# Performance work log

Hardware: AMD Instinct MI355X
Metric: run time of the kernel (lower is better)

Reference implementation:

```python
import jax, jax.numpy as jnp
import numpy as np

IN_FEATURES = 4096
OUT_FEATURES = 4096
N_OUTLIERS = 40
NBITS = 8


def setup_inputs() -> dict:
    key = jax.random.key(0)
    k1, k2, k3, k4 = jax.random.split(key, 4)
    x = jax.random.normal(k1, (4, 2048, IN_FEATURES), dtype=jnp.float32)
    weight = jax.random.normal(k2, (OUT_FEATURES, IN_FEATURES), dtype=jnp.float32)
    B = jax.random.normal(k3, (OUT_FEATURES, N_OUTLIERS), dtype=jnp.float32)
    bias = jax.random.normal(k4, (1, OUT_FEATURES), dtype=jnp.float32)
    # evenly spread outlier channel indices (as from_float would pick hot channels)
    outlier_idx = (jnp.arange(N_OUTLIERS, dtype=jnp.int32) * 102).astype(jnp.int32)
    return {"x": x, "weight": weight, "B": B, "bias": bias, "outlier_idx": outlier_idx}


def _uniform_quant(t, n_bits=NBITS):
    q_max = 2 ** (n_bits - 1) - 1  # 127 for 8 bits
    scale = jnp.maximum(jnp.max(jnp.abs(t)), 1e-5) / q_max
    return jnp.round(t / scale) * scale


def reference(x, weight, B, bias, outlier_idx):
    # abs-max over non-outlier channels only (mask out outlier columns)
    mask = jnp.ones((IN_FEATURES,), dtype=x.dtype).at[outlier_idx].set(0.0)
    upper = jnp.max(jnp.abs(x) * mask)
    x_clip = jnp.clip(x, -upper, upper)
    # outlier residual: part of x clipped away on the outlier channels
    x_outlier = jnp.take(x, outlier_idx, axis=-1) - jnp.take(x_clip, outlier_idx, axis=-1)
    res_y = jnp.einsum('bsk,ok->bso', x_outlier, B)  # skinny GEMM [*,40] x [40,out]
    # fake-quantize clipped activations, then main GEMM
    q_x = _uniform_quant(x_clip)
    y = jnp.einsum('bsi,oi->bso', q_x, weight) + bias
    # quantize_output=False -> no_quant on y
    return y + res_y
```

## Files before the change

kernel.cpp:

```cpp
#include <hip/hip_runtime.h>
#include <hip/hip_bf16.h>
#include <stdint.h>

#define IN_F 4096
#define OUT_F 4096
#define NOUT 40
#define KPAD 4160
#define M_TOT 8192

#define BM 256
#define BN 256
#define BK 64
#define KTILES 65

typedef float f32x4 __attribute__((ext_vector_type(4)));
typedef __bf16 bf16x8 __attribute__((ext_vector_type(8)));

typedef __attribute__((address_space(1))) void GV;
typedef __attribute__((address_space(3))) void LV;
#define GLDS16(gp, lp) \
  __builtin_amdgcn_global_load_lds((GV*)(gp), (LV*)(lp), 16, 0, 0)

__device__ __forceinline__ unsigned short f2bf(float f) {
  unsigned u = __float_as_uint(f);
  u += 0x7FFFu + ((u >> 16) & 1u);
  return (unsigned short)(u >> 16);
}

__global__ void k_absmax(const float4* __restrict__ x4, const int* __restrict__ oidx,
                         unsigned* __restrict__ out) {
  __shared__ unsigned bits[128];
  const int t = threadIdx.x;
  if (t < 128) bits[t] = 0;
  __syncthreads();
  if (t < NOUT) {
    int c = oidx[t];
    atomicOr(&bits[c >> 5], 1u << (c & 31));
  }
  __syncthreads();
  const int n4 = M_TOT * IN_F / 4;
  float m = 0.f;
  const int stride = gridDim.x * blockDim.x;
  for (int i = blockIdx.x * blockDim.x + t; i < n4; i += stride) {
    float4 u = x4[i];
    unsigned wb = bits[(i & 1023) >> 3];
    int sh = (i & 7) * 4;
    m = fmaxf(m, ((wb >> (sh + 0)) & 1) ? 0.f : fabsf(u.x));
    m = fmaxf(m, ((wb >> (sh + 1)) & 1) ? 0.f : fabsf(u.y));
    m = fmaxf(m, ((wb >> (sh + 2)) & 1) ? 0.f : fabsf(u.z));
    m = fmaxf(m, ((wb >> (sh + 3)) & 1) ? 0.f : fabsf(u.w));
  }
#pragma unroll
  for (int off = 32; off; off >>= 1) m = fmaxf(m, __shfl_down(m, off, 64));
  if ((t & 63) == 0) atomicMax(out, __float_as_uint(m));
}

__global__ void k_prep_a(const float* __restrict__ x,
                         const int* __restrict__ oidx,
                         const unsigned* __restrict__ upper_bits,
                         unsigned short* __restrict__ A) {
  const int m = blockIdx.x;
  const int t = threadIdx.x;
  const float upper = __uint_as_float(*upper_bits);
  const float inv = 127.0f / fmaxf(upper, 1e-5f);
  const float4* xr = (const float4*)(x + (size_t)m * IN_F);
  uint4* Ar = (uint4*)(A + (size_t)m * KPAD);
#pragma unroll
  for (int rep = 0; rep < 2; ++rep) {
    const int c = t + rep * 256;
    float4 u0 = xr[2 * c];
    float4 u1 = xr[2 * c + 1];
    float f[8] = {u0.x, u0.y, u0.z, u0.w, u1.x, u1.y, u1.z, u1.w};
    unsigned o[4];
#pragma unroll
    for (int w = 0; w < 4; ++w) {
      float a = fminf(fmaxf(f[2 * w], -upper), upper);
      float b = fminf(fmaxf(f[2 * w + 1], -upper), upper);
      unsigned short b0 = f2bf(rintf(a * inv));
      unsigned short b1 = f2bf(rintf(b * inv));
      o[w] = (unsigned)b0 | ((unsigned)b1 << 16);
    }
    uint4 ov; ov.x = o[0]; ov.y = o[1]; ov.z = o[2]; ov.w = o[3];
    Ar[c] = ov;
  }
  if (t < 64) {
    unsigned short v = 0;
    if (t < NOUT) {
      float xf = x[(size_t)m * IN_F + oidx[t]];
      float xc = fminf(fmaxf(xf, -upper), upper);
      v = f2bf((xf - xc) * inv);
    }
    A[(size_t)m * KPAD + IN_F + t] = v;
  }
}

__global__ void k_prep_w(const float* __restrict__ w, const float* __restrict__ Bm,
                         unsigned short* __restrict__ W) {
  const int o = blockIdx.x;
  const int t = threadIdx.x;
  const float4* wr = (const float4*)(w + (size_t)o * IN_F);
  uint4* Wr = (uint4*)(W + (size_t)o * KPAD);
#pragma unroll
  for (int rep = 0; rep < 2; ++rep) {
    const int c = t + rep * 256;
    float4 u0 = wr[2 * c];
    float4 u1 = wr[2 * c + 1];
    uint4 ov;
    ov.x = (unsigned)f2bf(u0.x) | ((unsigned)f2bf(u0.y) << 16);
    ov.y = (unsigned)f2bf(u0.z) | ((unsigned)f2bf(u0.w) << 16);
    ov.z = (unsigned)f2bf(u1.x) | ((unsigned)f2bf(u1.y) << 16);
    ov.w = (unsigned)f2bf(u1.z) | ((unsigned)f2bf(u1.w) << 16);
    Wr[c] = ov;
  }
  if (t < 64)
    W[(size_t)o * KPAD + IN_F + t] =
        (t < NOUT) ? f2bf(Bm[(size_t)o * NOUT + t]) : (unsigned short)0;
}

__global__ __launch_bounds__(512, 2) void k_gemm(
    const unsigned short* __restrict__ A, const unsigned short* __restrict__ W,
    const float* __restrict__ bias, const unsigned* __restrict__ upper_bits,
    float* __restrict__ out) {
  __shared__ __attribute__((aligned(16))) unsigned short As[2][BM * BK];
  __shared__ __attribute__((aligned(16))) unsigned short Ws[2][BN * BK];

  const int t = threadIdx.x;

  const int wg = ((int)blockIdx.x & 7) * 64 + ((int)blockIdx.x >> 3);
  const int bm = (wg >> 4) * BM;
  const int bn = (wg & 15) * BN;

  const int lane = t & 63;
  const int wave = t >> 6;
  const int wm = (wave >> 2) * 128;
  const int wn = (wave & 3) * 64;
  const int lrow = lane & 15, lquad = lane >> 4;

  f32x4 acc[8][4] = {};

  const int kswz = (((t & 7) ^ ((t >> 3) & 7)) * 8);
  const unsigned short* Ag = A + (size_t)(bm + (t >> 3)) * KPAD + kswz;
  const unsigned short* Wg = W + (size_t)(bn + (t >> 3)) * KPAD + kswz;
  char* ldsA0 = (char*)&As[0][0] + t * 16;
  char* ldsA1 = (char*)&As[1][0] + t * 16;
  char* ldsW0 = (char*)&Ws[0][0] + t * 16;
  char* ldsW1 = (char*)&Ws[1][0] + t * 16;
  const size_t rstep = (size_t)64 * KPAD;

#define STAGE_TILE(lA, lW, k0)                      \
  do {                                              \
    GLDS16(Ag + (k0), (lA));                        \
    GLDS16(Ag + (k0) + rstep, (lA) + 8192);         \
    GLDS16(Ag + (k0) + 2 * rstep, (lA) + 16384);    \
    GLDS16(Ag + (k0) + 3 * rstep, (lA) + 24576);    \
    GLDS16(Wg + (k0), (lW));                        \
    GLDS16(Wg + (k0) + rstep, (lW) + 8192);         \
    GLDS16(Wg + (k0) + 2 * rstep, (lW) + 16384);    \
    GLDS16(Wg + (k0) + 3 * rstep, (lW) + 24576);    \
  } while (0)

  const int x7 = lrow & 7;
  const int s0 = ((lquad) ^ x7) * 8;
  const int s1 = ((4 + lquad) ^ x7) * 8;

  STAGE_TILE(ldsA0, ldsW0, 0);
  STAGE_TILE(ldsA1, ldsW1, BK);
  asm volatile("s_waitcnt vmcnt(8)\n\ts_barrier" ::: "memory");

  for (int j = 0; j < KTILES; ++j) {
    const int b = j & 1;
    const unsigned short* Ab = b ? &As[1][0] : &As[0][0];
    const unsigned short* Wb = b ? &Ws[1][0] : &Ws[0][0];

    bf16x8 av[8][2], bv[4][2];
#pragma unroll
    for (int c = 0; c < 2; ++c) {
      const int sc = c ? s1 : s0;
#pragma unroll
      for (int jj = 0; jj < 4; ++jj)
        bv[jj][c] = *(const bf16x8*)(Wb + (wn + jj * 16 + lrow) * BK + sc);
#pragma unroll
      for (int ii = 0; ii < 8; ++ii)
        av[ii][c] = *(const bf16x8*)(Ab + (wm + ii * 16 + lrow) * BK + sc);
    }

    if (j < KTILES - 2) {
      asm volatile("s_waitcnt lgkmcnt(0)\n\ts_barrier" ::: "memory");
      char* lA = b ? ldsA1 : ldsA0;
      char* lW = b ? ldsW1 : ldsW0;
      STAGE_TILE(lA, lW, (j + 2) * BK);
    }

    __builtin_amdgcn_s_setprio(1);
#pragma unroll
    for (int c = 0; c < 2; ++c)
#pragma unroll
      for (int ii = 0; ii < 8; ++ii)
#pragma unroll
        for (int jj = 0; jj < 4; ++jj)
          acc[ii][jj] = __builtin_amdgcn_mfma_f32_16x16x32_bf16(
              av[ii][c], bv[jj][c], acc[ii][jj], 0, 0, 0);
    __builtin_amdgcn_s_setprio(0);

    if (j < KTILES - 2) {
      asm volatile("s_waitcnt vmcnt(8)\n\ts_barrier" ::: "memory");
    } else if (j == KTILES - 2) {
      asm volatile("s_waitcnt vmcnt(0)\n\ts_barrier" ::: "memory");
    }
  }
#undef STAGE_TILE

  const float scale = fmaxf(__uint_as_float(*upper_bits), 1e-5f) * (1.0f / 127.0f);
#pragma unroll
  for (int ii = 0; ii < 8; ++ii) {
    const int row = bm + wm + ii * 16 + lquad * 4;
#pragma unroll
    for (int jj = 0; jj < 4; ++jj) {
      const int col = bn + wn + jj * 16 + lrow;
      const float bs = bias[col];
#pragma unroll
      for (int r = 0; r < 4; ++r)
        out[(size_t)(row + r) * OUT_F + col] = scale * acc[ii][jj][r] + bs;
    }
  }
}

extern "C" void kernel_launch(void* const* d_in, const int* in_sizes, int n_in,
                              void* d_out, int out_size, void* d_ws, size_t ws_size,
                              hipStream_t stream) {
  (void)in_sizes; (void)n_in; (void)out_size; (void)ws_size;
  const float* x    = (const float*)d_in[0];
  const float* w    = (const float*)d_in[1];
  const float* B    = (const float*)d_in[2];
  const float* bias = (const float*)d_in[3];
  const int* oidx   = (const int*)d_in[4];
  float* out = (float*)d_out;

  char* ws = (char*)d_ws;
  unsigned* upper = (unsigned*)ws;
  unsigned short* Ap = (unsigned short*)(ws + 65536);
  unsigned short* Wp = Ap + (size_t)M_TOT * KPAD;

  hipMemsetAsync(upper, 0, 4, stream);
  k_absmax<<<2048, 256, 0, stream>>>((const float4*)x, oidx, upper);
  k_prep_a<<<M_TOT, 256, 0, stream>>>(x, oidx, upper, Ap);
  k_prep_w<<<OUT_F, 256, 0, stream>>>(w, B, Wp);
  k_gemm<<<(M_TOT / BM) * (OUT_F / BN), 512, 0, stream>>>(Ap, Wp, bias, upper, out);
}
```

Before: 615.2 us.

## Fuse absmax with weight prep and split GEMM K-loop into four staged phases

Merges the activation abs-max reduction and the weight bf16 conversion into one launch, so the two independent prep jobs share a grid and one launch is dropped. Restructures the GEMM main loop into four sub-phases per K-tile. Each phase interleaves LDS fragment reads, partial global-to-LDS staging and a quarter of the MFMAs, with A prefetched one tile ahead and W two tiles ahead in half-tile chunks. The aim is to overlap memory traffic with matrix math at finer grain. In exchange it adds extra barriers per tile, and the staging order needs correct vmcnt accounting.

```diff
diff --git a/kernel.cpp b/kernel.cpp
--- a/kernel.cpp
+++ b/kernel.cpp
@@ -12,6 +12,7 @@
 #define BN 256
 #define BK 64
 #define KTILES 65
+#define ABS_BLOCKS 2048
 
 typedef float f32x4 __attribute__((ext_vector_type(4)));
 typedef __bf16 bf16x8 __attribute__((ext_vector_type(8)));
@@ -27,32 +28,57 @@
   return (unsigned short)(u >> 16);
 }
 
-__global__ void k_absmax(const float4* __restrict__ x4, const int* __restrict__ oidx,
-                         unsigned* __restrict__ out) {
+__global__ void k_absmax_prepw(const float4* __restrict__ x4,
+                               const int* __restrict__ oidx,
+                               unsigned* __restrict__ out,
+                               const float* __restrict__ w,
+                               const float* __restrict__ Bm,
+                               unsigned short* __restrict__ W) {
   __shared__ unsigned bits[128];
   const int t = threadIdx.x;
-  if (t < 128) bits[t] = 0;
-  __syncthreads();
-  if (t < NOUT) {
-    int c = oidx[t];
-    atomicOr(&bits[c >> 5], 1u << (c & 31));
-  }
-  __syncthreads();
-  const int n4 = M_TOT * IN_F / 4;
-  float m = 0.f;
-  const int stride = gridDim.x * blockDim.x;
-  for (int i = blockIdx.x * blockDim.x + t; i < n4; i += stride) {
-    float4 u = x4[i];
-    unsigned wb = bits[(i & 1023) >> 3];
-    int sh = (i & 7) * 4;
-    m = fmaxf(m, ((wb >> (sh + 0)) & 1) ? 0.f : fabsf(u.x));
-    m = fmaxf(m, ((wb >> (sh + 1)) & 1) ? 0.f : fabsf(u.y));
-    m = fmaxf(m, ((wb >> (sh + 2)) & 1) ? 0.f : fabsf(u.z));
-    m = fmaxf(m, ((wb >> (sh + 3)) & 1) ? 0.f : fabsf(u.w));
-  }
-#pragma unroll
-  for (int off = 32; off; off >>= 1) m = fmaxf(m, __shfl_down(m, off, 64));
-  if ((t & 63) == 0) atomicMax(out, __float_as_uint(m));
+  if ((int)blockIdx.x < ABS_BLOCKS) {
+    if (t < 128) bits[t] = 0;
+    __syncthreads();
+    if (t < NOUT) {
+      int c = oidx[t];
+      atomicOr(&bits[c >> 5], 1u << (c & 31));
+    }
+    __syncthreads();
+    const int n4 = M_TOT * IN_F / 4;
+    float m = 0.f;
+    const int stride = ABS_BLOCKS * 256;
+    for (int i = blockIdx.x * 256 + t; i < n4; i += stride) {
+      float4 u = x4[i];
+      unsigned wb = bits[(i & 1023) >> 3];
+      int sh = (i & 7) * 4;
+      m = fmaxf(m, ((wb >> (sh + 0)) & 1) ? 0.f : fabsf(u.x));
+      m = fmaxf(m, ((wb >> (sh + 1)) & 1) ? 0.f : fabsf(u.y));
+      m = fmaxf(m, ((wb >> (sh + 2)) & 1) ? 0.f : fabsf(u.z));
+      m = fmaxf(m, ((wb >> (sh + 3)) & 1) ? 0.f : fabsf(u.w));
+    }
+#pragma unroll
+    for (int off = 32; off; off >>= 1) m = fmaxf(m, __shfl_down(m, off, 64));
+    if ((t & 63) == 0) atomicMax(out, __float_as_uint(m));
+  } else {
+    const int o = (int)blockIdx.x - ABS_BLOCKS;
+    const float4* wr = (const float4*)(w + (size_t)o * IN_F);
+    uint4* Wr = (uint4*)(W + (size_t)o * KPAD);
+#pragma unroll
+    for (int rep = 0; rep < 2; ++rep) {
+      const int c = t + rep * 256;
+      float4 u0 = wr[2 * c];
+      float4 u1 = wr[2 * c + 1];
+      uint4 ov;
+      ov.x = (unsigned)f2bf(u0.x) | ((unsigned)f2bf(u0.y) << 16);
+      ov.y = (unsigned)f2bf(u0.z) | ((unsigned)f2bf(u0.w) << 16);
+      ov.z = (unsigned)f2bf(u1.x) | ((unsigned)f2bf(u1.y) << 16);
+      ov.w = (unsigned)f2bf(u1.z) | ((unsigned)f2bf(u1.w) << 16);
+      Wr[c] = ov;
+    }
+    if (t < 64)
+      W[(size_t)o * KPAD + IN_F + t] =
+          (t < NOUT) ? f2bf(Bm[(size_t)o * NOUT + t]) : (unsigned short)0;
+  }
 }
 
 __global__ void k_prep_a(const float* __restrict__ x,
@@ -94,35 +120,12 @@
   }
 }
 
-__global__ void k_prep_w(const float* __restrict__ w, const float* __restrict__ Bm,
-                         unsigned short* __restrict__ W) {
-  const int o = blockIdx.x;
-  const int t = threadIdx.x;
-  const float4* wr = (const float4*)(w + (size_t)o * IN_F);
-  uint4* Wr = (uint4*)(W + (size_t)o * KPAD);
-#pragma unroll
-  for (int rep = 0; rep < 2; ++rep) {
-    const int c = t + rep * 256;
-    float4 u0 = wr[2 * c];
-    float4 u1 = wr[2 * c + 1];
-    uint4 ov;
-    ov.x = (unsigned)f2bf(u0.x) | ((unsigned)f2bf(u0.y) << 16);
-    ov.y = (unsigned)f2bf(u0.z) | ((unsigned)f2bf(u0.w) << 16);
-    ov.z = (unsigned)f2bf(u1.x) | ((unsigned)f2bf(u1.y) << 16);
-    ov.w = (unsigned)f2bf(u1.z) | ((unsigned)f2bf(u1.w) << 16);
-    Wr[c] = ov;
-  }
-  if (t < 64)
-    W[(size_t)o * KPAD + IN_F + t] =
-        (t < NOUT) ? f2bf(Bm[(size_t)o * NOUT + t]) : (unsigned short)0;
-}
-
 __global__ __launch_bounds__(512, 2) void k_gemm(
     const unsigned short* __restrict__ A, const unsigned short* __restrict__ W,
     const float* __restrict__ bias, const unsigned* __restrict__ upper_bits,
     float* __restrict__ out) {
-  __shared__ __attribute__((aligned(16))) unsigned short As[2][BM * BK];
-  __shared__ __attribute__((aligned(16))) unsigned short Ws[2][BN * BK];
+  __shared__ __attribute__((aligned(16))) unsigned short As[2][2][128][64];
+  __shared__ __attribute__((aligned(16))) unsigned short Ws[2][2][128][64];
 
   const int t = threadIdx.x;
 
@@ -135,80 +138,111 @@
   const int wm = (wave >> 2) * 128;
   const int wn = (wave & 3) * 64;
   const int lrow = lane & 15, lquad = lane >> 4;
+  const int x7 = lrow & 7;
+  const int hA = wm >> 7;
+  const int hW = wn >> 7;
+  const int rW0 = wn & 64;
 
   f32x4 acc[8][4] = {};
 
   const int kswz = (((t & 7) ^ ((t >> 3) & 7)) * 8);
   const unsigned short* Ag = A + (size_t)(bm + (t >> 3)) * KPAD + kswz;
   const unsigned short* Wg = W + (size_t)(bn + (t >> 3)) * KPAD + kswz;
-  char* ldsA0 = (char*)&As[0][0] + t * 16;
-  char* ldsA1 = (char*)&As[1][0] + t * 16;
-  char* ldsW0 = (char*)&Ws[0][0] + t * 16;
-  char* ldsW1 = (char*)&Ws[1][0] + t * 16;
-  const size_t rstep = (size_t)64 * KPAD;
-
-#define STAGE_TILE(lA, lW, k0)                      \
-  do {                                              \
-    GLDS16(Ag + (k0), (lA));                        \
-    GLDS16(Ag + (k0) + rstep, (lA) + 8192);         \
-    GLDS16(Ag + (k0) + 2 * rstep, (lA) + 16384);    \
-    GLDS16(Ag + (k0) + 3 * rstep, (lA) + 24576);    \
-    GLDS16(Wg + (k0), (lW));                        \
-    GLDS16(Wg + (k0) + rstep, (lW) + 8192);         \
-    GLDS16(Wg + (k0) + 2 * rstep, (lW) + 16384);    \
-    GLDS16(Wg + (k0) + 3 * rstep, (lW) + 24576);    \
-  } while (0)
-
-  const int x7 = lrow & 7;
-  const int s0 = ((lquad) ^ x7) * 8;
-  const int s1 = ((4 + lquad) ^ x7) * 8;
-
-  STAGE_TILE(ldsA0, ldsW0, 0);
-  STAGE_TILE(ldsA1, ldsW1, BK);
-  asm volatile("s_waitcnt vmcnt(8)\n\ts_barrier" ::: "memory");
+
+  const unsigned short* Asf = &As[0][0][0][0];
+  const unsigned short* Wsf = &Ws[0][0][0][0];
+
+#define STAGE_A(q, dbuf, kk) \
+  GLDS16(Ag + (size_t)(q) * 64 * KPAD + (kk), (char*)As + (dbuf) * 32768 + (q) * 8192 + t * 16)
+#define STAGE_W(q, dbuf, kk) \
+  GLDS16(Wg + (size_t)(q) * 64 * KPAD + (kk), (char*)Ws + (dbuf) * 32768 + (q) * 8192 + t * 16)
+
+#define LDA(b, ii, c) (*(const bf16x8*)(Asf + \
+    (((b) * 2 + hA) * 128 + (ii) * 16 + lrow) * 64 + ((((c) * 4 + lquad) ^ x7) * 8)))
+#define LDW(b, jj, c) (*(const bf16x8*)(Wsf + \
+    (((b) * 2 + hW) * 128 + rW0 + (jj) * 16 + lrow) * 64 + ((((c) * 4 + lquad) ^ x7) * 8)))
+
+#define PHASE_OPEN                                         \
+  __builtin_amdgcn_s_barrier();                            \
+  asm volatile("s_waitcnt lgkmcnt(0)" ::: "memory");       \
+  __builtin_amdgcn_sched_barrier(0)
+
+  STAGE_A(0, 0, 0); STAGE_A(1, 0, 0); STAGE_A(2, 0, 0); STAGE_A(3, 0, 0);
+  STAGE_W(0, 0, 0); STAGE_W(1, 0, 0); STAGE_W(2, 0, 0); STAGE_W(3, 0, 0);
+  STAGE_W(0, 1, BK); STAGE_W(1, 1, BK); STAGE_W(2, 1, BK); STAGE_W(3, 1, BK);
+  asm volatile("s_waitcnt vmcnt(4)" ::: "memory");
+  __builtin_amdgcn_s_barrier();
 
   for (int j = 0; j < KTILES; ++j) {
     const int b = j & 1;
-    const unsigned short* Ab = b ? &As[1][0] : &As[0][0];
-    const unsigned short* Wb = b ? &Ws[1][0] : &Ws[0][0];
-
-    bf16x8 av[8][2], bv[4][2];
-#pragma unroll
-    for (int c = 0; c < 2; ++c) {
-      const int sc = c ? s1 : s0;
-#pragma unroll
-      for (int jj = 0; jj < 4; ++jj)
-        bv[jj][c] = *(const bf16x8*)(Wb + (wn + jj * 16 + lrow) * BK + sc);
-#pragma unroll
-      for (int ii = 0; ii < 8; ++ii)
-        av[ii][c] = *(const bf16x8*)(Ab + (wm + ii * 16 + lrow) * BK + sc);
-    }
-
-    if (j < KTILES - 2) {
-      asm volatile("s_waitcnt lgkmcnt(0)\n\ts_barrier" ::: "memory");
-      char* lA = b ? ldsA1 : ldsA0;
-      char* lW = b ? ldsW1 : ldsW0;
-      STAGE_TILE(lA, lW, (j + 2) * BK);
-    }
-
-    __builtin_amdgcn_s_setprio(1);
-#pragma unroll
-    for (int c = 0; c < 2; ++c)
-#pragma unroll
-      for (int ii = 0; ii < 8; ++ii)
-#pragma unroll
-        for (int jj = 0; jj < 4; ++jj)
-          acc[ii][jj] = __builtin_amdgcn_mfma_f32_16x16x32_bf16(
-              av[ii][c], bv[jj][c], acc[ii][jj], 0, 0, 0);
-    __builtin_amdgcn_s_setprio(0);
-
-    if (j < KTILES - 2) {
-      asm volatile("s_waitcnt vmcnt(8)\n\ts_barrier" ::: "memory");
-    } else if (j == KTILES - 2) {
-      asm volatile("s_waitcnt vmcnt(0)\n\ts_barrier" ::: "memory");
-    }
-  }
-#undef STAGE_TILE
+    const int bA = b ^ 1;
+    const int kA = (j < KTILES - 1 ? j + 1 : KTILES - 1) * BK;
+    const int kW = (j < KTILES - 2 ? j + 2 : KTILES - 1) * BK;
+    bf16x8 aLo[4], aHi[4], b0[4], b1[4];
+
+#pragma unroll
+    for (int ii = 0; ii < 4; ++ii) aLo[ii] = LDA(b, ii, 0);
+#pragma unroll
+    for (int jj = 0; jj < 4; ++jj) b0[jj] = LDW(b, jj, 0);
+    STAGE_A(0, bA, kA); STAGE_A(2, bA, kA);
+    PHASE_OPEN;
+    __builtin_amdgcn_s_setprio(1);
+#pragma unroll
+    for (int ii = 0; ii < 4; ++ii)
+#pragma unroll
+      for (int jj = 0; jj < 4; ++jj)
+        acc[ii][jj] = __builtin_amdgcn_mfma_f32_16x16x32_bf16(aLo[ii], b0[jj], acc[ii][jj], 0, 0, 0);
+    __builtin_amdgcn_s_setprio(0);
+    __builtin_amdgcn_s_barrier();
+
+#pragma unroll
+    for (int jj = 0; jj < 4; ++jj) b1[jj] = LDW(b, jj, 1);
+#pragma unroll
+    for (int ii = 0; ii < 4; ++ii) aHi[ii] = LDA(b, ii + 4, 0);
+    STAGE_A(1, bA, kA); STAGE_A(3, bA, kA);
+    PHASE_OPEN;
+    __builtin_amdgcn_s_setprio(1);
+#pragma unroll
+    for (int ii = 0; ii < 4; ++ii)
+#pragma unroll
+      for (int jj = 0; jj < 4; ++jj)
+        acc[ii + 4][jj] = __builtin_amdgcn_mfma_f32_16x16x32_bf16(aHi[ii], b0[jj], acc[ii + 4][jj], 0, 0, 0);
+    __builtin_amdgcn_s_setprio(0);
+    __builtin_amdgcn_s_barrier();
+
+#pragma unroll
+    for (int ii = 0; ii < 4; ++ii) aLo[ii] = LDA(b, ii, 1);
+    STAGE_W(0, b, kW); STAGE_W(1, b, kW);
+    PHASE_OPEN;
+    __builtin_amdgcn_s_setprio(1);
+#pragma unroll
+    for (int ii = 0; ii < 4; ++ii)
+#pragma unroll
+      for (int jj = 0; jj < 4; ++jj)
+        acc[ii][jj] = __builtin_amdgcn_mfma_f32_16x16x32_bf16(aLo[ii], b1[jj], acc[ii][jj], 0, 0, 0);
+    __builtin_amdgcn_s_setprio(0);
+    __builtin_amdgcn_s_barrier();
+
+#pragma unroll
+    for (int ii = 0; ii < 4; ++ii) aHi[ii] = LDA(b, ii + 4, 1);
+    STAGE_W(2, b, kW); STAGE_W(3, b, kW);
+    PHASE_OPEN;
+    __builtin_amdgcn_s_setprio(1);
+#pragma unroll
+    for (int ii = 0; ii < 4; ++ii)
+#pragma unroll
+      for (int jj = 0; jj < 4; ++jj)
+        acc[ii + 4][jj] = __builtin_amdgcn_mfma_f32_16x16x32_bf16(aHi[ii], b1[jj], acc[ii + 4][jj], 0, 0, 0);
+    __builtin_amdgcn_s_setprio(0);
+    asm volatile("s_waitcnt vmcnt(4)" ::: "memory");
+    __builtin_amdgcn_s_barrier();
+  }
+  asm volatile("s_waitcnt vmcnt(0)" ::: "memory");
+#undef STAGE_A
+#undef STAGE_W
+#undef LDA
+#undef LDW
+#undef PHASE_OPEN
 
   const float scale = fmaxf(__uint_as_float(*upper_bits), 1e-5f) * (1.0f / 127.0f);
 #pragma unroll
@@ -242,8 +276,8 @@
   unsigned short* Wp = Ap + (size_t)M_TOT * KPAD;
 
   hipMemsetAsync(upper, 0, 4, stream);
-  k_absmax<<<2048, 256, 0, stream>>>((const float4*)x, oidx, upper);
+  k_absmax_prepw<<<ABS_BLOCKS + OUT_F, 256, 0, stream>>>(
+      (const float4*)x, oidx, upper, w, B, Wp);
   k_prep_a<<<M_TOT, 256, 0, stream>>>(x, oidx, upper, Ap);
-  k_prep_w<<<OUT_F, 256, 0, stream>>>(w, B, Wp);
   k_gemm<<<(M_TOT / BM) * (OUT_F / BN), 512, 0, stream>>>(Ap, Wp, bias, upper, out);
 }
```

Result: slower. 711.2 us (+15.6%).

## Fuse absmax reduction with weight prep and replace atomics with two-pass reduction

Applied to the files above, without the earlier changes.

Merges the activation abs-max reduction and the weight bf16 conversion into one kernel launch whose block ranges do different work, so both memory-bound passes run concurrently. The global atomicMax and memset are replaced with per-block partial maxima reduced by a small finalize kernel. This removes one launch and the memset and overlaps two bandwidth-bound phases, but adds a tiny extra kernel and lowers the absmax grid to 1024 blocks.

```diff
diff --git a/kernel.cpp b/kernel.cpp
--- a/kernel.cpp
+++ b/kernel.cpp
@@ -12,6 +12,7 @@
 #define BN 256
 #define BK 64
 #define KTILES 65
+#define ABS_BLOCKS 1024
 
 typedef float f32x4 __attribute__((ext_vector_type(4)));
 typedef __bf16 bf16x8 __attribute__((ext_vector_type(8)));
@@ -27,32 +28,77 @@
   return (unsigned short)(u >> 16);
 }
 
-__global__ void k_absmax(const float4* __restrict__ x4, const int* __restrict__ oidx,
-                         unsigned* __restrict__ out) {
+__global__ void k_absmax_prepw(const float4* __restrict__ x4,
+                               const int* __restrict__ oidx,
+                               float* __restrict__ partial,
+                               const float* __restrict__ w,
+                               const float* __restrict__ Bm,
+                               unsigned short* __restrict__ W) {
   __shared__ unsigned bits[128];
-  const int t = threadIdx.x;
-  if (t < 128) bits[t] = 0;
+  __shared__ float wmax[4];
+  const int t = threadIdx.x;
+  if ((int)blockIdx.x < ABS_BLOCKS) {
+    if (t < 128) bits[t] = 0;
+    __syncthreads();
+    if (t < NOUT) {
+      int c = oidx[t];
+      atomicOr(&bits[c >> 5], 1u << (c & 31));
+    }
+    __syncthreads();
+    const int n4 = M_TOT * IN_F / 4;
+    float m = 0.f;
+    const int stride = ABS_BLOCKS * 256;
+    for (int i = blockIdx.x * 256 + t; i < n4; i += stride) {
+      float4 u = x4[i];
+      unsigned wb = bits[(i & 1023) >> 3];
+      int sh = (i & 7) * 4;
+      m = fmaxf(m, ((wb >> (sh + 0)) & 1) ? 0.f : fabsf(u.x));
+      m = fmaxf(m, ((wb >> (sh + 1)) & 1) ? 0.f : fabsf(u.y));
+      m = fmaxf(m, ((wb >> (sh + 2)) & 1) ? 0.f : fabsf(u.z));
+      m = fmaxf(m, ((wb >> (sh + 3)) & 1) ? 0.f : fabsf(u.w));
+    }
+#pragma unroll
+    for (int off = 32; off; off >>= 1) m = fmaxf(m, __shfl_down(m, off, 64));
+    if ((t & 63) == 0) wmax[t >> 6] = m;
+    __syncthreads();
+    if (t == 0)
+      partial[blockIdx.x] =
+          fmaxf(fmaxf(wmax[0], wmax[1]), fmaxf(wmax[2], wmax[3]));
+  } else {
+    const int o = (int)blockIdx.x - ABS_BLOCKS;
+    const float4* wr = (const float4*)(w + (size_t)o * IN_F);
+    uint4* Wr = (uint4*)(W + (size_t)o * KPAD);
+#pragma unroll
+    for (int rep = 0; rep < 2; ++rep) {
+      const int c = t + rep * 256;
+      float4 u0 = wr[2 * c];
+      float4 u1 = wr[2 * c + 1];
+      uint4 ov;
+      ov.x = (unsigned)f2bf(u0.x) | ((unsigned)f2bf(u0.y) << 16);
+      ov.y = (unsigned)f2bf(u0.z) | ((unsigned)f2bf(u0.w) << 16);
+      ov.z = (unsigned)f2bf(u1.x) | ((unsigned)f2bf(u1.y) << 16);
+      ov.w = (unsigned)f2bf(u1.z) | ((unsigned)f2bf(u1.w) << 16);
+      Wr[c] = ov;
+    }
+    if (t < 64)
+      W[(size_t)o * KPAD + IN_F + t] =
+          (t < NOUT) ? f2bf(Bm[(size_t)o * NOUT + t]) : (unsigned short)0;
+  }
+}
+
+__global__ void k_finalize(const float* __restrict__ partial,
+                           unsigned* __restrict__ out) {
+  __shared__ float wmax[4];
+  const int t = threadIdx.x;
+  float m = 0.f;
+  for (int i = t; i < ABS_BLOCKS; i += 256) m = fmaxf(m, partial[i]);
+#pragma unroll
+  for (int off = 32; off; off >>= 1) m = fmaxf(m, __shfl_down(m, off, 64));
+  if ((t & 63) == 0) wmax[t >> 6] = m;
   __syncthreads();
-  if (t < NOUT) {
-    int c = oidx[t];
-    atomicOr(&bits[c >> 5], 1u << (c & 31));
-  }
-  __syncthreads();
-  const int n4 = M_TOT * IN_F / 4;
-  float m = 0.f;
-  const int stride = gridDim.x * blockDim.x;
-  for (int i = blockIdx.x * blockDim.x + t; i < n4; i += stride) {
-    float4 u = x4[i];
-    unsigned wb = bits[(i & 1023) >> 3];
-    int sh = (i & 7) * 4;
-    m = fmaxf(m, ((wb >> (sh + 0)) & 1) ? 0.f : fabsf(u.x));
-    m = fmaxf(m, ((wb >> (sh + 1)) & 1) ? 0.f : fabsf(u.y));
-    m = fmaxf(m, ((wb >> (sh + 2)) & 1) ? 0.f : fabsf(u.z));
-    m = fmaxf(m, ((wb >> (sh + 3)) & 1) ? 0.f : fabsf(u.w));
-  }
-#pragma unroll
-  for (int off = 32; off; off >>= 1) m = fmaxf(m, __shfl_down(m, off, 64));
-  if ((t & 63) == 0) atomicMax(out, __float_as_uint(m));
+  if (t == 0)
+    *out = __float_as_uint(
+        fmaxf(fmaxf(wmax[0], wmax[1]), fmaxf(wmax[2], wmax[3])));
 }
 
 __global__ void k_prep_a(const float* __restrict__ x,
@@ -92,29 +138,6 @@
     }
     A[(size_t)m * KPAD + IN_F + t] = v;
   }
-}
-
-__global__ void k_prep_w(const float* __restrict__ w, const float* __restrict__ Bm,
-                         unsigned short* __restrict__ W) {
-  const int o = blockIdx.x;
-  const int t = threadIdx.x;
-  const float4* wr = (const float4*)(w + (size_t)o * IN_F);
-  uint4* Wr = (uint4*)(W + (size_t)o * KPAD);
-#pragma unroll
-  for (int rep = 0; rep < 2; ++rep) {
-    const int c = t + rep * 256;
-    float4 u0 = wr[2 * c];
-    float4 u1 = wr[2 * c + 1];
-    uint4 ov;
-    ov.x = (unsigned)f2bf(u0.x) | ((unsigned)f2bf(u0.y) << 16);
-    ov.y = (unsigned)f2bf(u0.z) | ((unsigned)f2bf(u0.w) << 16);
-    ov.z = (unsigned)f2bf(u1.x) | ((unsigned)f2bf(u1.y) << 16);
-    ov.w = (unsigned)f2bf(u1.z) | ((unsigned)f2bf(u1.w) << 16);
-    Wr[c] = ov;
-  }
-  if (t < 64)
-    W[(size_t)o * KPAD + IN_F + t] =
-        (t < NOUT) ? f2bf(Bm[(size_t)o * NOUT + t]) : (unsigned short)0;
 }
 
 __global__ __launch_bounds__(512, 2) void k_gemm(
@@ -238,12 +261,13 @@
 
   char* ws = (char*)d_ws;
   unsigned* upper = (unsigned*)ws;
+  float* partial = (float*)(ws + 256);
   unsigned short* Ap = (unsigned short*)(ws + 65536);
   unsigned short* Wp = Ap + (size_t)M_TOT * KPAD;
 
-  hipMemsetAsync(upper, 0, 4, stream);
-  k_absmax<<<2048, 256, 0, stream>>>((const float4*)x, oidx, upper);
+  k_absmax_prepw<<<ABS_BLOCKS + OUT_F, 256, 0, stream>>>(
+      (const float4*)x, oidx, partial, w, B, Wp);
+  k_finalize<<<1, 256, 0, stream>>>(partial, upper);
   k_prep_a<<<M_TOT, 256, 0, stream>>>(x, oidx, upper, Ap);
-  k_prep_w<<<OUT_F, 256, 0, stream>>>(w, B, Wp);
   k_gemm<<<(M_TOT / BM) * (OUT_F / BN), 512, 0, stream>>>(Ap, Wp, bias, upper, out);
 }
```

Result: faster. 529.2 us (-14.0%).
